# Optimization experiments

Measured on AMD Instinct MI355X. Metric: run time of the kernel, lower is better.

Reference implementation:

```python
import math
import jax, jax.numpy as jnp
import numpy as np
from jax.scipy.special import gammaln, xlogy

HEADS = 8
DIM_KEY = 64
DIM_VALUE = 64
NUM_REL_POS_FEATURES = 192
DIM = 768
SEQ = 2048
BATCH = 2


def get_positional_embed(seq_len: int, feature_size: int) -> jnp.ndarray:
    # distances: [2n-1]
    distances = jnp.arange(-seq_len + 1, seq_len, dtype=jnp.float32)
    f = feature_size // 6  # 3 basis classes, then doubled with sign term
    absd = jnp.abs(distances)[:, None]  # [2n-1, 1]
    # exponential basis
    max_range = math.log(seq_len) / math.log(2.0)
    half_life = 2.0 ** jnp.linspace(3.0, max_range, f)[None, :]
    exp_feat = jnp.exp(-math.log(2.0) / half_life * absd)
    # central mask basis
    center_widths = 2.0 ** jnp.arange(1, f + 1, dtype=jnp.float32) - 1.0
    cmask = (center_widths[None, :] > absd).astype(jnp.float32)
    # gamma pdf basis
    stddev = seq_len / (2.0 * f)
    start_mean = seq_len / f
    mean = jnp.linspace(start_mean, float(seq_len), f)[None, :]
    concentration = (mean / stddev) ** 2
    rate = mean / stddev ** 2
    log_unnorm = xlogy(concentration - 1.0, absd) - rate * absd
    log_norm = gammaln(concentration) - concentration * jnp.log(rate)
    probs = jnp.exp(log_unnorm - log_norm) + 1e-8
    gamma_feat = probs / jnp.max(probs, axis=-1, keepdims=True)
    emb = jnp.concatenate([exp_feat, cmask, gamma_feat], axis=-1)  # [2n-1, 3f]
    return jnp.concatenate([emb, jnp.sign(distances)[:, None] * emb], axis=-1)  # [2n-1, 6f]


def relative_shift(x: jnp.ndarray) -> jnp.ndarray:
    # x: [b, h, n, 2n-1] -> [b, h, n, n] via Transformer-XL shift trick
    x = jnp.concatenate([jnp.zeros_like(x[..., :1]), x], axis=-1)
    b, h, t1, t2 = x.shape  # t2 = 2n
    x = x.reshape(b, h, t2, t1)[:, :, 1:, :].reshape(b, h, t1, t2 - 1)
    return x[..., : (t2 + 1) // 2]


def setup_inputs() -> dict:
    key = jax.random.key(0)
    ks = jax.random.split(key, 9)
    d_inner = HEADS * DIM_KEY
    d_vinner = HEADS * DIM_VALUE
    sc = 1.0 / math.sqrt(DIM)
    return {
        "x": jax.random.normal(ks[0], (BATCH, SEQ, DIM), dtype=jnp.float32),
        "Wq": jax.random.normal(ks[1], (DIM, d_inner), dtype=jnp.float32) * sc,
        "Wk": jax.random.normal(ks[2], (DIM, d_inner), dtype=jnp.float32) * sc,
        "Wv": jax.random.normal(ks[3], (DIM, d_vinner), dtype=jnp.float32) * sc,
        "Wrel": jax.random.normal(ks[4], (NUM_REL_POS_FEATURES, d_inner), dtype=jnp.float32) * (1.0 / math.sqrt(NUM_REL_POS_FEATURES)),
        "rel_content_bias": jax.random.normal(ks[5], (1, HEADS, 1, DIM_KEY), dtype=jnp.float32),
        "rel_pos_bias": jax.random.normal(ks[6], (1, HEADS, 1, DIM_KEY), dtype=jnp.float32),
        "Wo": jax.random.normal(ks[7], (d_vinner, DIM), dtype=jnp.float32) * (1.0 / math.sqrt(d_vinner)),
        "bo": jax.random.normal(ks[8], (DIM,), dtype=jnp.float32) * 0.01,
    }


def reference(x, Wq, Wk, Wv, Wrel, rel_content_bias, rel_pos_bias, Wo, bo):
    b, n, _ = x.shape
    scale = DIM_KEY ** -0.5
    # projections -> [b, h, n, d]
    q = (x @ Wq).reshape(b, n, HEADS, DIM_KEY).transpose(0, 2, 1, 3) * scale
    k = (x @ Wk).reshape(b, n, HEADS, DIM_KEY).transpose(0, 2, 1, 3)
    v = (x @ Wv).reshape(b, n, HEADS, DIM_VALUE).transpose(0, 2, 1, 3)
    content_logits = jnp.einsum("bhid,bhjd->bhij", q + rel_content_bias, k)
    positions = get_positional_embed(n, NUM_REL_POS_FEATURES)  # [2n-1, F]
    rel_k = (positions @ Wrel).reshape(2 * n - 1, HEADS, DIM_KEY).transpose(1, 0, 2)  # [h, 2n-1, d]
    rel_logits = jnp.einsum("bhid,hjd->bhij", q + rel_pos_bias, rel_k)
    rel_logits = relative_shift(rel_logits)  # [b, h, n, n]
    attn = jax.nn.softmax(content_logits + rel_logits, axis=-1)
    out = jnp.einsum("bhij,bhjd->bhid", attn, v)  # [b, h, n, dv]
    out = out.transpose(0, 2, 1, 3).reshape(b, n, HEADS * DIM_VALUE)
    return out @ Wo + bo
```

## Files before the change

### kernel.cpp

```cpp
#include <hip/hip_runtime.h>
#include <hip/hip_bf16.h>
#include <math.h>


typedef _Float16 f16x8 __attribute__((ext_vector_type(8)));
typedef _Float16 f16x4 __attribute__((ext_vector_type(4)));
typedef float f32x4 __attribute__((ext_vector_type(4)));

#define MFMA16(a, b, c) __builtin_amdgcn_mfma_f32_16x16x32_f16((a), (b), (c), 0, 0, 0)

#define GL16(gp, lp)                                                       \
  __builtin_amdgcn_global_load_lds(                                        \
      (const __attribute__((address_space(1))) void*)(gp),                 \
      (__attribute__((address_space(3))) void*)(lp), 16, 0, 0)

__device__ __forceinline__ float dpp_fmax16(float x) {
  int v;
  v = __builtin_amdgcn_update_dpp(0, __float_as_int(x), 0xB1, 0xf, 0xf, true);
  x = fmaxf(x, __int_as_float(v));
  v = __builtin_amdgcn_update_dpp(0, __float_as_int(x), 0x4E, 0xf, 0xf, true);
  x = fmaxf(x, __int_as_float(v));
  v = __builtin_amdgcn_update_dpp(0, __float_as_int(x), 0x141, 0xf, 0xf, true);
  x = fmaxf(x, __int_as_float(v));
  v = __builtin_amdgcn_update_dpp(0, __float_as_int(x), 0x140, 0xf, 0xf, true);
  x = fmaxf(x, __int_as_float(v));
  return x;
}

__global__ __launch_bounds__(256) void prep_kernel(
    const float* __restrict__ x, const float* __restrict__ Wq,
    const float* __restrict__ Wk, const float* __restrict__ Wv,
    const float* __restrict__ Wrel, const float* __restrict__ Wo,
    _Float16* __restrict__ xb, _Float16* __restrict__ wqkvt,
    _Float16* __restrict__ wrelt, _Float16* __restrict__ wot,
    _Float16* __restrict__ posb) {
  __shared__ float tile[32][33];
  const int t = threadIdx.x;
  int bid = blockIdx.x;
  if (bid < 3072) {
    const int idx = bid * 256 + t;
    float4 v = ((const float4*)x)[idx];
    f16x4 o;
    o[0] = (_Float16)v.x; o[1] = (_Float16)v.y; o[2] = (_Float16)v.z; o[3] = (_Float16)v.w;
    ((f16x4*)xb)[idx] = o;
    return;
  }
  bid -= 3072;
  if (bid < 1632) {
    const float* in; _Float16* out; int K_, N_, bx, by;
    if (bid < 1152) {
      const int z = bid / 384, rem = bid % 384;
      in = (z == 0) ? Wq : (z == 1) ? Wk : Wv;
      out = wqkvt + (size_t)z * 512 * 768;
      K_ = 768; N_ = 512; bx = rem & 15; by = rem >> 4;
    } else if (bid < 1248) {
      const int rem = bid - 1152;
      in = Wrel; out = wrelt;
      K_ = 192; N_ = 512; bx = rem & 15; by = rem >> 4;
    } else {
      const int rem = bid - 1248;
      in = Wo; out = wot;
      K_ = 512; N_ = 768; bx = rem % 24; by = rem / 24;
    }
    const int k0 = by * 32, n0 = bx * 32;
    const int tr = t >> 3, tc = (t & 7) * 4;
    float4 v = *(const float4*)(in + (size_t)(k0 + tr) * N_ + n0 + tc);
    tile[tr][tc] = v.x; tile[tr][tc + 1] = v.y; tile[tr][tc + 2] = v.z; tile[tr][tc + 3] = v.w;
    __syncthreads();
    f16x4 o;
    o[0] = (_Float16)tile[tc][tr];
    o[1] = (_Float16)tile[tc + 1][tr];
    o[2] = (_Float16)tile[tc + 2][tr];
    o[3] = (_Float16)tile[tc + 3][tr];
    *(f16x4*)(out + (size_t)(n0 + tr) * K_ + k0 + tc) = o;
    return;
  }
  bid -= 1632;
  const int lr = t >> 5, i = t & 31;
  const int r = bid * 8 + lr;
  _Float16* row = posb + (size_t)r * 192;
  if (r >= 4095) {
    row[i] = (_Float16)0.f; row[32 + i] = (_Float16)0.f; row[64 + i] = (_Float16)0.f;
    row[96 + i] = (_Float16)0.f; row[128 + i] = (_Float16)0.f; row[160 + i] = (_Float16)0.f;
    return;
  }
  const float dist = (float)(r - 2047);
  const float absd = fabsf(dist);
  const float sgn = (dist > 0.f) ? 1.f : ((dist < 0.f) ? -1.f : 0.f);
  const float e = 3.f + (float)i * (8.f / 31.f);
  const float expv = exp2f(-absd * exp2f(-e));
  const float cw = exp2f((float)(i + 1)) - 1.f;
  const float cm = (cw > absd) ? 1.f : 0.f;
  const float mean = 64.f * (float)(i + 1);
  const float conc = (mean / 32.f) * (mean / 32.f);
  const float rate = mean / 1024.f;
  const float lnrm = lgammaf(conc) - conc * logf(rate);
  const float lu = (conc - 1.f) * logf(absd) - rate * absd;
  float gv = expf(lu - lnrm) + 1e-8f;
  float mx = gv;
  mx = fmaxf(mx, __shfl_xor(mx, 1));
  mx = fmaxf(mx, __shfl_xor(mx, 2));
  mx = fmaxf(mx, __shfl_xor(mx, 4));
  mx = fmaxf(mx, __shfl_xor(mx, 8));
  mx = fmaxf(mx, __shfl_xor(mx, 16));
  gv /= mx;
  row[i] = (_Float16)expv;              row[32 + i] = (_Float16)cm;
  row[64 + i] = (_Float16)gv;           row[96 + i] = (_Float16)(sgn * expv);
  row[128 + i] = (_Float16)(sgn * cm);  row[160 + i] = (_Float16)(sgn * gv);
}

template <int MODE>
__global__ __launch_bounds__(256, 4) void gemm_tile(
    const _Float16* __restrict__ A, const _Float16* __restrict__ Bt,
    const int N, const int K,
    _Float16* __restrict__ o0, _Float16* __restrict__ o1,
    _Float16* __restrict__ o2, _Float16* __restrict__ o3,
    const float* __restrict__ bias0, const float* __restrict__ bias1,
    float* __restrict__ outf) {
  __shared__ __align__(16) _Float16 As[2][64 * 32];
  __shared__ __align__(16) _Float16 Bs[2][128 * 32];
  const int tid = threadIdx.x;
  const int w = tid >> 6, lane = tid & 63, g = lane >> 4, m = lane & 15;
  const int wr = w >> 1, wc = w & 1;
  const int row0 = blockIdx.y * 64;
  const int c0 = blockIdx.x * 128;

  const int arow = tid >> 2, asl = tid & 3;
  const int axor = asl ^ ((arow >> 1) & 3);
  const char* Ag = (const char*)(A + (size_t)(row0 + arow) * K) + (axor << 4);
  const int adst = (arow << 6) + (asl << 4);
  const int brow = w * 32 + (lane >> 2);
  const int bxor = asl ^ ((brow >> 1) & 3);
  const char* Bg = (const char*)(Bt + (size_t)(c0 + brow) * K) + (bxor << 4);
  const size_t bstep = (size_t)16 * K * 2;
  const int bdst = (brow << 6) + (asl << 4);

  int aoff[2], boff[4];
#pragma unroll
  for (int i = 0; i < 2; ++i) {
    const int ar = wr * 32 + i * 16 + m;
    aoff[i] = (ar << 6) + ((g ^ ((ar >> 1) & 3)) << 4);
  }
#pragma unroll
  for (int i = 0; i < 4; ++i) {
    const int br = wc * 64 + i * 16 + m;
    boff[i] = (br << 6) + ((g ^ ((br >> 1) & 3)) << 4);
  }

#define STAGEG(buf, k0v)                                       \
  GL16(Ag + ((k0v) << 1), (char*)As[buf] + adst);              \
  GL16(Bg + ((k0v) << 1), (char*)Bs[buf] + bdst);              \
  GL16(Bg + bstep + ((k0v) << 1), (char*)Bs[buf] + bdst + 1024);

  f32x4 acc[2][4] = {};
  STAGEG(0, 0);
  __syncthreads();
  const int nk = K >> 5;
  for (int ks = 0; ks < nk; ++ks) {
    const int cur = ks & 1;
    if (ks + 1 < nk) { STAGEG(cur ^ 1, (ks + 1) << 5); }
    const char* ap = (const char*)As[cur];
    const char* bp = (const char*)Bs[cur];
    f16x8 af[2], bf[4];
#pragma unroll
    for (int i = 0; i < 2; ++i) af[i] = *(const f16x8*)(ap + aoff[i]);
#pragma unroll
    for (int i = 0; i < 4; ++i) bf[i] = *(const f16x8*)(bp + boff[i]);
#pragma unroll
    for (int mi = 0; mi < 2; ++mi)
#pragma unroll
      for (int ni = 0; ni < 4; ++ni)
        acc[mi][ni] = MFMA16(af[mi], bf[ni], acc[mi][ni]);
    __syncthreads();
  }
#undef STAGEG

  const int proj = (MODE == 0) ? (c0 >> 9) : 0;
#pragma unroll
  for (int ni = 0; ni < 4; ++ni) {
    const int col = c0 + wc * 64 + ni * 16 + m;
    const int c = col & 511, hh = (MODE == 0) ? (c >> 6) : (col >> 6);
    const int dk = col & 63;
    float b0f = 0.f, b1f = 0.f;
    if (MODE == 0 && proj == 0) { b0f = bias0[c]; b1f = bias1[c]; }
    if (MODE == 0 && proj == 2) {
#pragma unroll
      for (int mi = 0; mi < 2; ++mi) {
        const int rowb = row0 + wr * 32 + mi * 16 + g * 4;
        const int bb = rowb >> 11, n = rowb & 2047;
        f16x4 pk;
#pragma unroll
        for (int r = 0; r < 4; ++r) pk[r] = (_Float16)acc[mi][ni][r];
        *(f16x4*)(o3 + ((size_t)(bb * 8 + hh) * 64 + dk) * 2048 + n) = pk;
      }
    } else {
#pragma unroll
      for (int mi = 0; mi < 2; ++mi) {
#pragma unroll
        for (int r = 0; r < 4; ++r) {
          const int row = row0 + wr * 32 + mi * 16 + g * 4 + r;
          const float v = acc[mi][ni][r];
          if (MODE == 0) {
            const int bb = row >> 11, n = row & 2047;
            const size_t ad = ((size_t)(bb * 8 + hh) * 2048 + n) * 64 + dk;
            if (proj == 0) {
              const float vs = v * 0.125f;
              o0[ad] = (_Float16)(vs + b0f);
              o1[ad] = (_Float16)(vs + b1f);
            } else {
              o2[ad] = (_Float16)v;
            }
          } else if (MODE == 3) {
            o0[((size_t)hh * 4096 + row) * 64 + dk] = (_Float16)v;
          } else {
            outf[(size_t)row * N + col] = v + bias0[col];
          }
        }
      }
    }
  }
}

__global__ __launch_bounds__(256, 2) void attn_kernel(
    const _Float16* __restrict__ qc, const _Float16* __restrict__ qp,
    const _Float16* __restrict__ kb, const _Float16* __restrict__ vtb,
    const _Float16* __restrict__ relkb, _Float16* __restrict__ attnb) {
  __shared__ __align__(16) char lds[2 * 32768 + 4 * 2304];
  const int tid = threadIdx.x;
  const int w = tid >> 6, lane = tid & 63, g = lane >> 4, m = lane & 15;
  const int L = blockIdx.x;
  const int h = L & 7;
  const int r2 = L >> 3;
  const int b = r2 >> 5, xt = r2 & 31;
  const int bh = b * 8 + h;
  const int i0b = xt << 6;
  const int i0 = i0b + w * 16;

  const int srow = tid >> 3, ssl = tid & 7;
  const int sxr16 = (ssl ^ (srow & 7)) << 4;
  const int dst16 = (srow << 7) + (ssl << 4);
  const char* kgs = (const char*)kb + ((size_t)bh << 18) + sxr16;
  const char* vgs = (const char*)vtb + ((size_t)bh << 18) + ((size_t)srow << 12) + sxr16;
  const char* rgs = (const char*)relkb + ((size_t)h << 19) + sxr16;

#define STAGE(halfp, j0v, d0v)                                                  \
  GL16(kgs + ((size_t)((j0v) + srow) << 7), (halfp) + dst16);                   \
  GL16(kgs + ((size_t)((j0v) + srow + 32) << 7), (halfp) + dst16 + 4096);       \
  GL16(vgs + ((j0v) << 1), (halfp) + 8192 + dst16);                             \
  GL16(vgs + ((size_t)32 << 12) + ((j0v) << 1), (halfp) + 8192 + dst16 + 4096); \
  GL16(rgs + ((size_t)((d0v) + srow) << 7), (halfp) + 16384 + dst16);           \
  GL16(rgs + ((size_t)((d0v) + srow + 32) << 7), (halfp) + 16384 + dst16 + 4096); \
  GL16(rgs + ((size_t)((d0v) + srow + 64) << 7), (halfp) + 16384 + dst16 + 8192); \
  GL16(rgs + ((size_t)((d0v) + srow + 96) << 7), (halfp) + 16384 + dst16 + 12288);

  STAGE(lds, 0, 1984 - i0b);

  const size_t qbase = ((size_t)bh * 2048 + i0 + m) * 64 + g * 8;
  f16x8 qcf0 = *(const f16x8*)(qc + qbase);
  f16x8 qcf1 = *(const f16x8*)(qc + qbase + 32);
  f16x8 qpf0 = *(const f16x8*)(qp + qbase);
  f16x8 qpf1 = *(const f16x8*)(qp + qbase + 32);

  f16x8 onesv;
#pragma unroll
  for (int i = 0; i < 8; ++i) onesv[i] = (_Float16)1.f;

  __syncthreads();

  f32x4 acc_o[4] = {};
  f32x4 acc_l = {};
  float m_run[4];
#pragma unroll
  for (int r = 0; r < 4; ++r) m_run[r] = -1e30f;

  const int sx = m & 7;
  const int fo0 = (g ^ sx) << 4;
  const int fo1 = ((4 | g) ^ sx) << 4;
  const int rrow0 = 48 - (w << 4) + m;
  _Float16* Pl = (_Float16*)(lds + 65536 + w * 2304);

  for (int jt = 0; jt < 32; ++jt) {
    if (jt < 31) {
      const int j0n = (jt + 1) << 6;
      char* nh = lds + (((jt & 1) ^ 1) << 15);
      STAGE(nh, j0n, j0n - i0b + 1984);
    }
    const char* curh = lds + ((jt & 1) << 15);
    f32x4 sc[4] = {};
#pragma unroll
    for (int cf = 0; cf < 4; ++cf) {
      const char* kp = curh + ((m + (cf << 4)) << 7);
      sc[cf] = MFMA16(qcf0, *(const f16x8*)(kp + fo0), sc[cf]);
      sc[cf] = MFMA16(qcf1, *(const f16x8*)(kp + fo1), sc[cf]);
    }
    f32x4 rc[5] = {};
#pragma unroll
    for (int cf = 0; cf < 5; ++cf) {
      const char* rp = curh + 16384 + ((rrow0 + (cf << 4)) << 7);
      rc[cf] = MFMA16(qpf0, *(const f16x8*)(rp + fo0), rc[cf]);
      rc[cf] = MFMA16(qpf1, *(const f16x8*)(rp + fo1), rc[cf]);
    }
#pragma unroll
    for (int r = 0; r < 4; ++r) {
      const int lr = g * 4 + r;
      const int u = 15 + m - lr;
      const int src = (g << 4) | (u & 15);
      const bool hi = (m > lr);
      float sh0 = __shfl(rc[0][r], src);
      float sh1 = __shfl(rc[1][r], src);
      float sh2 = __shfl(rc[2][r], src);
      float sh3 = __shfl(rc[3][r], src);
      float sh4 = __shfl(rc[4][r], src);
      sc[0][r] += hi ? sh1 : sh0;
      sc[1][r] += hi ? sh2 : sh1;
      sc[2][r] += hi ? sh3 : sh2;
      sc[3][r] += hi ? sh4 : sh3;
    }
    float P[4][4];
#pragma unroll
    for (int r = 0; r < 4; ++r) {
      float mx = fmaxf(fmaxf(sc[0][r], sc[1][r]), fmaxf(sc[2][r], sc[3][r]));
      mx = dpp_fmax16(mx);
      const float mnew = fmaxf(m_run[r], mx);
      const float corr = __expf(m_run[r] - mnew);
      m_run[r] = mnew;
#pragma unroll
      for (int cf = 0; cf < 4; ++cf) {
        P[cf][r] = __expf(sc[cf][r] - mnew);
        acc_o[cf][r] *= corr;
      }
      acc_l[r] *= corr;
    }
#pragma unroll
    for (int cf = 0; cf < 4; ++cf)
#pragma unroll
      for (int r = 0; r < 4; ++r)
        Pl[(g * 4 + r) * 72 + cf * 16 + m] = (_Float16)P[cf][r];
#pragma unroll
    for (int ks = 0; ks < 2; ++ks) {
      f16x8 pa = *(const f16x8*)((const char*)Pl + m * 144 + ks * 64 + (g << 4));
#pragma unroll
      for (int cf = 0; cf < 4; ++cf) {
        const char* vp = curh + 8192 + ((m + (cf << 4)) << 7);
        acc_o[cf] = MFMA16(pa, *(const f16x8*)(vp + (ks ? fo1 : fo0)), acc_o[cf]);
      }
      acc_l = MFMA16(pa, onesv, acc_l);
    }
    __syncthreads();
  }
#pragma unroll
  for (int cf = 0; cf < 4; ++cf)
#pragma unroll
    for (int r = 0; r < 4; ++r) {
      const int i = i0 + g * 4 + r;
      const float o = acc_o[cf][r] / acc_l[r];
      attnb[((size_t)(b * 2048 + i)) * 512 + h * 64 + cf * 16 + m] = (_Float16)o;
    }
#undef STAGE
}

extern "C" void kernel_launch(void* const* d_in, const int* in_sizes, int n_in,
                              void* d_out, int out_size, void* d_ws, size_t ws_size,
                              hipStream_t stream) {
  (void)in_sizes; (void)n_in; (void)out_size; (void)ws_size;
  const float* x    = (const float*)d_in[0];
  const float* Wq   = (const float*)d_in[1];
  const float* Wk   = (const float*)d_in[2];
  const float* Wv   = (const float*)d_in[3];
  const float* Wrel = (const float*)d_in[4];
  const float* bc   = (const float*)d_in[5];
  const float* bp   = (const float*)d_in[6];
  const float* Wo   = (const float*)d_in[7];
  const float* bo   = (const float*)d_in[8];
  float* out = (float*)d_out;

  char* ws = (char*)d_ws;
  size_t off = 0;
  auto alloc = [&](size_t bytes) -> void* {
    void* p = ws + off;
    off += (bytes + 255) & ~(size_t)255;
    return p;
  };
  _Float16* xb     = (_Float16*)alloc(4096ull * 768 * 2);
  _Float16* wqkvt  = (_Float16*)alloc(1536ull * 768 * 2);
  _Float16* wrelt  = (_Float16*)alloc(512ull * 192 * 2);
  _Float16* wot    = (_Float16*)alloc(768ull * 512 * 2);
  _Float16* posb   = (_Float16*)alloc(4096ull * 192 * 2);
  _Float16* qcb    = (_Float16*)alloc(16ull * 2048 * 64 * 2);
  _Float16* qpb    = (_Float16*)alloc(16ull * 2048 * 64 * 2);
  _Float16* kbb    = (_Float16*)alloc(16ull * 2048 * 64 * 2);
  _Float16* vtb    = (_Float16*)alloc(16ull * 64 * 2048 * 2);
  _Float16* relkb  = (_Float16*)alloc(8ull * 4096 * 64 * 2);
  _Float16* attnb  = (_Float16*)alloc(4096ull * 512 * 2);

  prep_kernel<<<5216, 256, 0, stream>>>(x, Wq, Wk, Wv, Wrel, Wo,
                                        xb, wqkvt, wrelt, wot, posb);

  gemm_tile<0><<<dim3(12, 64), 256, 0, stream>>>(xb, wqkvt, 1536, 768,
                                                 qcb, qpb, kbb, vtb, bc, bp, nullptr);
  gemm_tile<3><<<dim3(4, 64), 256, 0, stream>>>(posb, wrelt, 512, 192,
                                                relkb, nullptr, nullptr, nullptr,
                                                nullptr, nullptr, nullptr);

  attn_kernel<<<512, 256, 0, stream>>>(qcb, qpb, kbb, vtb, relkb, attnb);

  gemm_tile<4><<<dim3(6, 64), 256, 0, stream>>>(attnb, wot, 768, 512,
                                                nullptr, nullptr, nullptr, nullptr,
                                                bo, nullptr, out);
}
```

Before: 191.5 us.

## Merge QKV and rel GEMMs, ring-buffer rel keys, lazy softmax rescale in attention

The QKV and relative-position GEMMs now run as one launch instead of two, and the output GEMM becomes its own specialized kernel. In the attention kernel, the relative-key tiles go through a three-slot ring, so each step stages only one new 64-row chunk instead of 128 rows. V is read directly from global memory rather than staged in LDS, which shrinks LDS use and allows 3 blocks per CU. The kernel also adds s_setprio around the MFMA sections and only rescales the running output when the row max grows by more than 8. Reading V from global adds latency to the PV step, and the lazy rescale relies on fp32 headroom to avoid overflow.

Measured after the change: 220.4 us. 1.15x slower.

```diff
diff --git a/kernel.cpp b/kernel.cpp
--- a/kernel.cpp
+++ b/kernel.cpp
@@ -109,21 +109,29 @@
   row[128 + i] = (_Float16)(sgn * cm);  row[160 + i] = (_Float16)(sgn * gv);
 }
 
-template <int MODE>
-__global__ __launch_bounds__(256, 4) void gemm_tile(
-    const _Float16* __restrict__ A, const _Float16* __restrict__ Bt,
-    const int N, const int K,
-    _Float16* __restrict__ o0, _Float16* __restrict__ o1,
-    _Float16* __restrict__ o2, _Float16* __restrict__ o3,
-    const float* __restrict__ bias0, const float* __restrict__ bias1,
-    float* __restrict__ outf) {
+__global__ __launch_bounds__(256, 4) void gemm_qkvrel(
+    const _Float16* __restrict__ xb, const _Float16* __restrict__ wqkvt,
+    const _Float16* __restrict__ posb, const _Float16* __restrict__ wrelt,
+    _Float16* __restrict__ qc, _Float16* __restrict__ qp,
+    _Float16* __restrict__ kbo, _Float16* __restrict__ vt,
+    _Float16* __restrict__ relk,
+    const float* __restrict__ bc, const float* __restrict__ bp) {
   __shared__ __align__(16) _Float16 As[2][64 * 32];
   __shared__ __align__(16) _Float16 Bs[2][128 * 32];
   const int tid = threadIdx.x;
   const int w = tid >> 6, lane = tid & 63, g = lane >> 4, m = lane & 15;
   const int wr = w >> 1, wc = w & 1;
-  const int row0 = blockIdx.y * 64;
-  const int c0 = blockIdx.x * 128;
+  const int bid = blockIdx.x;
+  const bool isrel = bid >= 768;
+  const _Float16* A; const _Float16* Bt; int K, row0, c0;
+  if (isrel) {
+    const int tt = bid - 768;
+    A = posb; Bt = wrelt; K = 192;
+    c0 = (tt & 3) * 128; row0 = (tt >> 2) * 64;
+  } else {
+    A = xb; Bt = wqkvt; K = 768;
+    c0 = (bid % 12) * 128; row0 = (bid / 12) * 64;
+  }
 
   const int arow = tid >> 2, asl = tid & 3;
   const int axor = asl ^ ((arow >> 1) & 3);
@@ -160,12 +168,12 @@
     const int cur = ks & 1;
     if (ks + 1 < nk) { STAGEG(cur ^ 1, (ks + 1) << 5); }
     const char* ap = (const char*)As[cur];
-    const char* bp = (const char*)Bs[cur];
+    const char* bp_ = (const char*)Bs[cur];
     f16x8 af[2], bf[4];
 #pragma unroll
     for (int i = 0; i < 2; ++i) af[i] = *(const f16x8*)(ap + aoff[i]);
 #pragma unroll
-    for (int i = 0; i < 4; ++i) bf[i] = *(const f16x8*)(bp + boff[i]);
+    for (int i = 0; i < 4; ++i) bf[i] = *(const f16x8*)(bp_ + boff[i]);
 #pragma unroll
     for (int mi = 0; mi < 2; ++mi)
 #pragma unroll
@@ -175,57 +183,140 @@
   }
 #undef STAGEG
 
-  const int proj = (MODE == 0) ? (c0 >> 9) : 0;
+  if (isrel) {
+#pragma unroll
+    for (int ni = 0; ni < 4; ++ni) {
+      const int col = c0 + wc * 64 + ni * 16 + m;
+      const int hh = col >> 6, dk = col & 63;
+#pragma unroll
+      for (int mi = 0; mi < 2; ++mi)
+#pragma unroll
+        for (int r = 0; r < 4; ++r) {
+          const int row = row0 + wr * 32 + mi * 16 + g * 4 + r;
+          relk[((size_t)hh * 4096 + row) * 64 + dk] = (_Float16)acc[mi][ni][r];
+        }
+    }
+  } else {
+    const int proj = c0 >> 9;
+#pragma unroll
+    for (int ni = 0; ni < 4; ++ni) {
+      const int col = c0 + wc * 64 + ni * 16 + m;
+      const int c = col & 511, hh = c >> 6, dk = c & 63;
+      float b0f = 0.f, b1f = 0.f;
+      if (proj == 0) { b0f = bc[c]; b1f = bp[c]; }
+      if (proj == 2) {
+#pragma unroll
+        for (int mi = 0; mi < 2; ++mi) {
+          const int rowb = row0 + wr * 32 + mi * 16 + g * 4;
+          const int bb = rowb >> 11, n = rowb & 2047;
+          f16x4 pk;
+#pragma unroll
+          for (int r = 0; r < 4; ++r) pk[r] = (_Float16)acc[mi][ni][r];
+          *(f16x4*)(vt + ((size_t)(bb * 8 + hh) * 64 + dk) * 2048 + n) = pk;
+        }
+      } else {
+#pragma unroll
+        for (int mi = 0; mi < 2; ++mi)
+#pragma unroll
+          for (int r = 0; r < 4; ++r) {
+            const int row = row0 + wr * 32 + mi * 16 + g * 4 + r;
+            const int bb = row >> 11, n = row & 2047;
+            const size_t ad = ((size_t)(bb * 8 + hh) * 2048 + n) * 64 + dk;
+            const float v = acc[mi][ni][r];
+            if (proj == 0) {
+              const float vs = v * 0.125f;
+              qc[ad] = (_Float16)(vs + b0f);
+              qp[ad] = (_Float16)(vs + b1f);
+            } else {
+              kbo[ad] = (_Float16)v;
+            }
+          }
+      }
+    }
+  }
+}
+
+__global__ __launch_bounds__(256, 4) void gemm_out(
+    const _Float16* __restrict__ A, const _Float16* __restrict__ Bt,
+    const float* __restrict__ bias, float* __restrict__ outf) {
+  __shared__ __align__(16) _Float16 As[2][64 * 32];
+  __shared__ __align__(16) _Float16 Bs[2][128 * 32];
+  const int tid = threadIdx.x;
+  const int w = tid >> 6, lane = tid & 63, g = lane >> 4, m = lane & 15;
+  const int wr = w >> 1, wc = w & 1;
+  const int K = 512;
+  const int row0 = blockIdx.y * 64;
+  const int c0 = blockIdx.x * 128;
+
+  const int arow = tid >> 2, asl = tid & 3;
+  const int axor = asl ^ ((arow >> 1) & 3);
+  const char* Ag = (const char*)(A + (size_t)(row0 + arow) * K) + (axor << 4);
+  const int adst = (arow << 6) + (asl << 4);
+  const int brow = w * 32 + (lane >> 2);
+  const int bxor = asl ^ ((brow >> 1) & 3);
+  const char* Bg = (const char*)(Bt + (size_t)(c0 + brow) * K) + (bxor << 4);
+  const size_t bstep = (size_t)16 * K * 2;
+  const int bdst = (brow << 6) + (asl << 4);
+
+  int aoff[2], boff[4];
+#pragma unroll
+  for (int i = 0; i < 2; ++i) {
+    const int ar = wr * 32 + i * 16 + m;
+    aoff[i] = (ar << 6) + ((g ^ ((ar >> 1) & 3)) << 4);
+  }
+#pragma unroll
+  for (int i = 0; i < 4; ++i) {
+    const int br = wc * 64 + i * 16 + m;
+    boff[i] = (br << 6) + ((g ^ ((br >> 1) & 3)) << 4);
+  }
+
+#define STAGEG(buf, k0v)                                       \
+  GL16(Ag + ((k0v) << 1), (char*)As[buf] + adst);              \
+  GL16(Bg + ((k0v) << 1), (char*)Bs[buf] + bdst);              \
+  GL16(Bg + bstep + ((k0v) << 1), (char*)Bs[buf] + bdst + 1024);
+
+  f32x4 acc[2][4] = {};
+  STAGEG(0, 0);
+  __syncthreads();
+  const int nk = K >> 5;
+  for (int ks = 0; ks < nk; ++ks) {
+    const int cur = ks & 1;
+    if (ks + 1 < nk) { STAGEG(cur ^ 1, (ks + 1) << 5); }
+    const char* ap = (const char*)As[cur];
+    const char* bp_ = (const char*)Bs[cur];
+    f16x8 af[2], bf[4];
+#pragma unroll
+    for (int i = 0; i < 2; ++i) af[i] = *(const f16x8*)(ap + aoff[i]);
+#pragma unroll
+    for (int i = 0; i < 4; ++i) bf[i] = *(const f16x8*)(bp_ + boff[i]);
+#pragma unroll
+    for (int mi = 0; mi < 2; ++mi)
+#pragma unroll
+      for (int ni = 0; ni < 4; ++ni)
+        acc[mi][ni] = MFMA16(af[mi], bf[ni], acc[mi][ni]);
+    __syncthreads();
+  }
+#undef STAGEG
+
 #pragma unroll
   for (int ni = 0; ni < 4; ++ni) {
     const int col = c0 + wc * 64 + ni * 16 + m;
-    const int c = col & 511, hh = (MODE == 0) ? (c >> 6) : (col >> 6);
-    const int dk = col & 63;
-    float b0f = 0.f, b1f = 0.f;
-    if (MODE == 0 && proj == 0) { b0f = bias0[c]; b1f = bias1[c]; }
-    if (MODE == 0 && proj == 2) {
-#pragma unroll
-      for (int mi = 0; mi < 2; ++mi) {
-        const int rowb = row0 + wr * 32 + mi * 16 + g * 4;
-        const int bb = rowb >> 11, n = rowb & 2047;
-        f16x4 pk;
-#pragma unroll
-        for (int r = 0; r < 4; ++r) pk[r] = (_Float16)acc[mi][ni][r];
-        *(f16x4*)(o3 + ((size_t)(bb * 8 + hh) * 64 + dk) * 2048 + n) = pk;
+    const float bv = bias[col];
+#pragma unroll
+    for (int mi = 0; mi < 2; ++mi)
+#pragma unroll
+      for (int r = 0; r < 4; ++r) {
+        const int row = row0 + wr * 32 + mi * 16 + g * 4 + r;
+        outf[(size_t)row * 768 + col] = acc[mi][ni][r] + bv;
       }
-    } else {
-#pragma unroll
-      for (int mi = 0; mi < 2; ++mi) {
-#pragma unroll
-        for (int r = 0; r < 4; ++r) {
-          const int row = row0 + wr * 32 + mi * 16 + g * 4 + r;
-          const float v = acc[mi][ni][r];
-          if (MODE == 0) {
-            const int bb = row >> 11, n = row & 2047;
-            const size_t ad = ((size_t)(bb * 8 + hh) * 2048 + n) * 64 + dk;
-            if (proj == 0) {
-              const float vs = v * 0.125f;
-              o0[ad] = (_Float16)(vs + b0f);
-              o1[ad] = (_Float16)(vs + b1f);
-            } else {
-              o2[ad] = (_Float16)v;
-            }
-          } else if (MODE == 3) {
-            o0[((size_t)hh * 4096 + row) * 64 + dk] = (_Float16)v;
-          } else {
-            outf[(size_t)row * N + col] = v + bias0[col];
-          }
-        }
-      }
-    }
   }
 }
 
-__global__ __launch_bounds__(256, 2) void attn_kernel(
+__global__ __launch_bounds__(256, 3) void attn_kernel(
     const _Float16* __restrict__ qc, const _Float16* __restrict__ qp,
     const _Float16* __restrict__ kb, const _Float16* __restrict__ vtb,
     const _Float16* __restrict__ relkb, _Float16* __restrict__ attnb) {
-  __shared__ __align__(16) char lds[2 * 32768 + 4 * 2304];
+  __shared__ __align__(16) char lds[50176];
   const int tid = threadIdx.x;
   const int w = tid >> 6, lane = tid & 63, g = lane >> 4, m = lane & 15;
   const int L = blockIdx.x;
@@ -235,25 +326,28 @@
   const int bh = b * 8 + h;
   const int i0b = xt << 6;
   const int i0 = i0b + w * 16;
+  const int dR = 1984 - i0b;
 
   const int srow = tid >> 3, ssl = tid & 7;
   const int sxr16 = (ssl ^ (srow & 7)) << 4;
   const int dst16 = (srow << 7) + (ssl << 4);
   const char* kgs = (const char*)kb + ((size_t)bh << 18) + sxr16;
-  const char* vgs = (const char*)vtb + ((size_t)bh << 18) + ((size_t)srow << 12) + sxr16;
   const char* rgs = (const char*)relkb + ((size_t)h << 19) + sxr16;
 
-#define STAGE(halfp, j0v, d0v)                                                  \
-  GL16(kgs + ((size_t)((j0v) + srow) << 7), (halfp) + dst16);                   \
-  GL16(kgs + ((size_t)((j0v) + srow + 32) << 7), (halfp) + dst16 + 4096);       \
-  GL16(vgs + ((j0v) << 1), (halfp) + 8192 + dst16);                             \
-  GL16(vgs + ((size_t)32 << 12) + ((j0v) << 1), (halfp) + 8192 + dst16 + 4096); \
-  GL16(rgs + ((size_t)((d0v) + srow) << 7), (halfp) + 16384 + dst16);           \
-  GL16(rgs + ((size_t)((d0v) + srow + 32) << 7), (halfp) + 16384 + dst16 + 4096); \
-  GL16(rgs + ((size_t)((d0v) + srow + 64) << 7), (halfp) + 16384 + dst16 + 8192); \
-  GL16(rgs + ((size_t)((d0v) + srow + 96) << 7), (halfp) + 16384 + dst16 + 12288);
-
-  STAGE(lds, 0, 1984 - i0b);
+  char* Kb0 = lds;
+  char* Kb1 = lds + 8192;
+  char* Ring = lds + 16384;
+
+#define STAGE_K(dstp, j0v)                                              \
+  GL16(kgs + ((size_t)((j0v) + srow) << 7), (dstp) + dst16);            \
+  GL16(kgs + ((size_t)((j0v) + srow + 32) << 7), (dstp) + dst16 + 4096);
+#define STAGE_R(dstp, c)                                                       \
+  GL16(rgs + ((size_t)(dR + ((c) << 6) + srow) << 7), (dstp) + dst16);         \
+  GL16(rgs + ((size_t)(dR + ((c) << 6) + srow + 32) << 7), (dstp) + dst16 + 4096);
+
+  STAGE_K(Kb0, 0);
+  STAGE_R(Ring, 0);
+  STAGE_R(Ring + 8192, 1);
 
   const size_t qbase = ((size_t)bh * 2048 + i0 + m) * 64 + g * 8;
   f16x8 qcf0 = *(const f16x8*)(qc + qbase);
@@ -276,30 +370,38 @@
   const int sx = m & 7;
   const int fo0 = (g ^ sx) << 4;
   const int fo1 = ((4 | g) ^ sx) << 4;
-  const int rrow0 = 48 - (w << 4) + m;
-  _Float16* Pl = (_Float16*)(lds + 65536 + w * 2304);
+  const int lb0 = 48 - (w << 4);
+  _Float16* Pl = (_Float16*)(lds + 40960 + w * 2304);
+
+  char* rsA = Ring;
+  char* rsB = Ring + 8192;
+  char* rsC = Ring + 16384;
 
   for (int jt = 0; jt < 32; ++jt) {
     if (jt < 31) {
-      const int j0n = (jt + 1) << 6;
-      char* nh = lds + (((jt & 1) ^ 1) << 15);
-      STAGE(nh, j0n, j0n - i0b + 1984);
-    }
-    const char* curh = lds + ((jt & 1) << 15);
+      char* kn = (jt & 1) ? Kb0 : Kb1;
+      STAGE_K(kn, (jt + 1) << 6);
+      STAGE_R(rsC, jt + 2);
+    }
+    const char* curK = (jt & 1) ? Kb1 : Kb0;
+    __builtin_amdgcn_s_setprio(1);
     f32x4 sc[4] = {};
 #pragma unroll
     for (int cf = 0; cf < 4; ++cf) {
-      const char* kp = curh + ((m + (cf << 4)) << 7);
+      const char* kp = curK + ((m + (cf << 4)) << 7);
       sc[cf] = MFMA16(qcf0, *(const f16x8*)(kp + fo0), sc[cf]);
       sc[cf] = MFMA16(qcf1, *(const f16x8*)(kp + fo1), sc[cf]);
     }
     f32x4 rc[5] = {};
 #pragma unroll
     for (int cf = 0; cf < 5; ++cf) {
-      const char* rp = curh + 16384 + ((rrow0 + (cf << 4)) << 7);
+      const int lb = lb0 + (cf << 4);
+      const char* sp = (lb & 64) ? rsB : rsA;
+      const char* rp = sp + (((lb & 63) + m) << 7);
       rc[cf] = MFMA16(qpf0, *(const f16x8*)(rp + fo0), rc[cf]);
       rc[cf] = MFMA16(qpf1, *(const f16x8*)(rp + fo1), rc[cf]);
     }
+    __builtin_amdgcn_s_setprio(0);
 #pragma unroll
     for (int r = 0; r < 4; ++r) {
       const int lr = g * 4 + r;
@@ -316,37 +418,51 @@
       sc[2][r] += hi ? sh3 : sh2;
       sc[3][r] += hi ? sh4 : sh3;
     }
+    float mx[4];
+#pragma unroll
+    for (int r = 0; r < 4; ++r) {
+      float v = fmaxf(fmaxf(sc[0][r], sc[1][r]), fmaxf(sc[2][r], sc[3][r]));
+      mx[r] = dpp_fmax16(v);
+    }
+    const bool need = (mx[0] > m_run[0] + 8.f) || (mx[1] > m_run[1] + 8.f) ||
+                      (mx[2] > m_run[2] + 8.f) || (mx[3] > m_run[3] + 8.f);
+    if (__any(need)) {
+#pragma unroll
+      for (int r = 0; r < 4; ++r) {
+        const float mnew = fmaxf(m_run[r], mx[r]);
+        const float corr = __expf(m_run[r] - mnew);
+        m_run[r] = mnew;
+#pragma unroll
+        for (int cf = 0; cf < 4; ++cf) acc_o[cf][r] *= corr;
+        acc_l[r] *= corr;
+      }
+    }
     float P[4][4];
 #pragma unroll
-    for (int r = 0; r < 4; ++r) {
-      float mx = fmaxf(fmaxf(sc[0][r], sc[1][r]), fmaxf(sc[2][r], sc[3][r]));
-      mx = dpp_fmax16(mx);
-      const float mnew = fmaxf(m_run[r], mx);
-      const float corr = __expf(m_run[r] - mnew);
-      m_run[r] = mnew;
-#pragma unroll
-      for (int cf = 0; cf < 4; ++cf) {
-        P[cf][r] = __expf(sc[cf][r] - mnew);
-        acc_o[cf][r] *= corr;
-      }
-      acc_l[r] *= corr;
-    }
+    for (int r = 0; r < 4; ++r)
+#pragma unroll
+      for (int cf = 0; cf < 4; ++cf)
+        P[cf][r] = __expf(sc[cf][r] - m_run[r]);
 #pragma unroll
     for (int cf = 0; cf < 4; ++cf)
 #pragma unroll
       for (int r = 0; r < 4; ++r)
         Pl[(g * 4 + r) * 72 + cf * 16 + m] = (_Float16)P[cf][r];
+    const size_t vbase = ((size_t)bh * 64 + m) * 2048 + ((size_t)jt << 6) + g * 8;
+    __builtin_amdgcn_s_setprio(1);
 #pragma unroll
     for (int ks = 0; ks < 2; ++ks) {
       f16x8 pa = *(const f16x8*)((const char*)Pl + m * 144 + ks * 64 + (g << 4));
 #pragma unroll
       for (int cf = 0; cf < 4; ++cf) {
-        const char* vp = curh + 8192 + ((m + (cf << 4)) << 7);
-        acc_o[cf] = MFMA16(pa, *(const f16x8*)(vp + (ks ? fo1 : fo0)), acc_o[cf]);
+        f16x8 vf = *(const f16x8*)(vtb + vbase + (size_t)cf * 32768 + ks * 32);
+        acc_o[cf] = MFMA16(pa, vf, acc_o[cf]);
       }
       acc_l = MFMA16(pa, onesv, acc_l);
     }
+    __builtin_amdgcn_s_setprio(0);
     __syncthreads();
+    char* tmp = rsA; rsA = rsB; rsB = rsC; rsC = tmp;
   }
 #pragma unroll
   for (int cf = 0; cf < 4; ++cf)
@@ -356,7 +472,8 @@
       const float o = acc_o[cf][r] / acc_l[r];
       attnb[((size_t)(b * 2048 + i)) * 512 + h * 64 + cf * 16 + m] = (_Float16)o;
     }
-#undef STAGE
+#undef STAGE_K
+#undef STAGE_R
 }
 
 extern "C" void kernel_launch(void* const* d_in, const int* in_sizes, int n_in,
@@ -396,15 +513,10 @@
   prep_kernel<<<5216, 256, 0, stream>>>(x, Wq, Wk, Wv, Wrel, Wo,
                                         xb, wqkvt, wrelt, wot, posb);
 
-  gemm_tile<0><<<dim3(12, 64), 256, 0, stream>>>(xb, wqkvt, 1536, 768,
-                                                 qcb, qpb, kbb, vtb, bc, bp, nullptr);
-  gemm_tile<3><<<dim3(4, 64), 256, 0, stream>>>(posb, wrelt, 512, 192,
-                                                relkb, nullptr, nullptr, nullptr,
-                                                nullptr, nullptr, nullptr);
+  gemm_qkvrel<<<1024, 256, 0, stream>>>(xb, wqkvt, posb, wrelt,
+                                        qcb, qpb, kbb, vtb, relkb, bc, bp);
 
   attn_kernel<<<512, 256, 0, stream>>>(qcb, qpb, kbb, vtb, relkb, attnb);
 
-  gemm_tile<4><<<dim3(6, 64), 256, 0, stream>>>(attnb, wot, 768, 512,
-                                                nullptr, nullptr, nullptr, nullptr,
-                                                bo, nullptr, out);
+  gemm_out<<<dim3(6, 64), 256, 0, stream>>>(attnb, wot, bo, out);
 }
```
